# Optimization experiments

Measured on AMD Instinct MI355X. Metric: run time of the kernel, lower is better.

## Reference

```python
import jax, jax.numpy as jnp
import numpy as np

B, T, C = 2, 2048, 1024
H, D = 16, 64


def setup_inputs() -> dict:
    key = jax.random.key(0)
    ks = jax.random.split(key, 5)
    s = 1.0 / np.sqrt(C)  # keep projections well-scaled
    return {
        "x": jax.random.normal(ks[0], (B, T, C), dtype=jnp.float32),
        "wq": jax.random.normal(ks[1], (C, C), dtype=jnp.float32) * s,
        "wk": jax.random.normal(ks[2], (C, C), dtype=jnp.float32) * s,
        "wv": jax.random.normal(ks[3], (C, C), dtype=jnp.float32) * s,
        "wo": jax.random.normal(ks[4], (C, C), dtype=jnp.float32) * s,
    }


def reference(x, wq, wk, wv, wo):
    # nn.Linear(d,d,bias=False): y = x @ W.T ; weights stored [out,in]
    q = (x @ wq.T).reshape(B, T, H, D).transpose(0, 2, 1, 3)  # [B,H,T,D]
    k = (x @ wk.T).reshape(B, T, H, D).transpose(0, 2, 1, 3)
    v = (x @ wv.T).reshape(B, T, H, D).transpose(0, 2, 1, 3)
    scale = jnp.sqrt(jnp.float32(D))
    scores = jnp.einsum("bhtd,bhsd->bhts", q, k) / scale  # [B,H,T,T]
    # additive causal mask: -inf above the diagonal
    causal = jnp.tril(jnp.ones((T, T), dtype=bool))
    scores = jnp.where(causal[None, None], scores, jnp.float32(-1e9))
    weights = jax.nn.softmax(scores, axis=-1)
    out = jnp.einsum("bhts,bhsd->bhtd", weights, v)  # [B,H,T,D]
    out = out.transpose(0, 2, 1, 3).reshape(B, T, C)
    return out @ wo.T
```

## Files before the change

kernel.cpp:

```cpp
#include <hip/hip_runtime.h>
#include <stdint.h>

#define B_ 2
#define T_ 2048
#define C_ 1024
#define H_ 16
#define D_ 64
#define M_ (B_*T_)

typedef __attribute__((ext_vector_type(8))) short bf16x8;
typedef __attribute__((ext_vector_type(4))) short bf16x4;
typedef __attribute__((ext_vector_type(4))) __bf16 bf16v4;
typedef __attribute__((ext_vector_type(4))) float f32x4;
typedef unsigned short u16;

#define MFMA32(a, b, c) __builtin_amdgcn_mfma_f32_16x16x32_bf16((a), (b), (c), 0, 0, 0)

__device__ __forceinline__ u16 f2bf(float f) {
  union { float f; uint32_t u; } v; v.f = f;
  uint32_t u = v.u;
  return (u16)((u + 0x7fffu + ((u >> 16) & 1u)) >> 16);
}

__device__ __forceinline__ float exp2_fast(float x) { return __builtin_amdgcn_exp2f(x); }

typedef const __attribute__((address_space(1))) void* gas_t;
typedef __attribute__((address_space(3))) void* las_t;
__device__ __forceinline__ void gld_lds16(const void* g, void* l) {
  __builtin_amdgcn_global_load_lds((gas_t)g, (las_t)l, 16, 0, 0);
}

__global__ void cvt_all(const float* __restrict__ x,
                        const float* __restrict__ w0, const float* __restrict__ w1,
                        const float* __restrict__ w2, const float* __restrict__ w3,
                        u16* __restrict__ xb,
                        u16* __restrict__ d0, u16* __restrict__ d1,
                        u16* __restrict__ d2, u16* __restrict__ d3) {
  size_t i = ((size_t)blockIdx.x * 256 + threadIdx.x) * 4;
  const float* s; u16* d; size_t off;
  const size_t NX = (size_t)M_ * C_;
  const size_t NW = (size_t)C_ * C_;
  if (i < NX) { s = x; d = xb; off = i; }
  else {
    size_t j = i - NX;
    int w = (int)(j / NW); off = j - (size_t)w * NW;
    switch (w) {
      case 0: s = w0; d = d0; break;
      case 1: s = w1; d = d1; break;
      case 2: s = w2; d = d2; break;
      default: s = w3; d = d3; break;
    }
  }
  float4 v = *(const float4*)(s + off);
  ushort4 o;
  o.x = f2bf(v.x); o.y = f2bf(v.y); o.z = f2bf(v.z); o.w = f2bf(v.w);
  *(ushort4*)(d + off) = o;
}

__device__ __forceinline__ void gemm_core(const u16* __restrict__ A,
                                          const u16* __restrict__ W,
                                          int m0, int n0, int Kt,
                                          f32x4 acc[4][4])
{
  __shared__ u16 As[128*64];
  __shared__ u16 Bs[128*64];
  const int t = threadIdx.x;
  const int lane = t & 63;
  const int wave = t >> 6;
  const int q = lane >> 4;
  const int l15 = lane & 15;
  const int wm = (wave >> 1) * 64;
  const int wn = (wave & 1) * 64;

  #pragma unroll
  for (int i = 0; i < 4; ++i)
    #pragma unroll
    for (int j = 0; j < 4; ++j)
      acc[i][j] = (f32x4){0.f, 0.f, 0.f, 0.f};

  for (int k0 = 0; k0 < Kt; k0 += 64) {
    #pragma unroll
    for (int r = 0; r < 4; ++r) {
      int Lc = r * 256 + t;
      int row = Lc >> 3;
      int gcc = (Lc & 7) ^ (row & 7);
      gld_lds16(A + (size_t)(m0 + row) * Kt + k0 + gcc * 8, As + Lc * 8);
    }
    #pragma unroll
    for (int r = 0; r < 4; ++r) {
      int Lc = r * 256 + t;
      int row = Lc >> 3;
      int gcc = (Lc & 7) ^ (row & 7);
      gld_lds16(W + (size_t)(n0 + row) * Kt + k0 + gcc * 8, Bs + Lc * 8);
    }
    __syncthreads();

    #pragma unroll
    for (int kk = 0; kk < 2; ++kk) {
      bf16x8 af[4], bfr[4];
      #pragma unroll
      for (int i = 0; i < 4; ++i) {
        int m = wm + i * 16 + l15;
        int ch = (kk * 4 + q) ^ (m & 7);
        af[i] = *(const bf16x8*)(As + m * 64 + ch * 8);
      }
      #pragma unroll
      for (int j = 0; j < 4; ++j) {
        int n = wn + j * 16 + l15;
        int ch = (kk * 4 + q) ^ (n & 7);
        bfr[j] = *(const bf16x8*)(Bs + n * 64 + ch * 8);
      }
      #pragma unroll
      for (int i = 0; i < 4; ++i)
        #pragma unroll
        for (int j = 0; j < 4; ++j)
          acc[i][j] = MFMA32(af[i], bfr[j], acc[i][j]);
    }
    __syncthreads();
  }
}

#define QSCALE 0.1803368801111244f
__global__ __launch_bounds__(256, 3)
void gemm_qkv(const u16* __restrict__ X,
              const u16* __restrict__ Wq, const u16* __restrict__ Wk,
              const u16* __restrict__ Wv,
              u16* __restrict__ Q, u16* __restrict__ K, u16* __restrict__ Vt)
{
  const int bm = blockIdx.x;
  const int bn = blockIdx.y;
  const int seg = bn >> 3;
  const int nb = (bn & 7) * 128;

  const int t = threadIdx.x, lane = t & 63, wave = t >> 6;
  const int q = lane >> 4, l15 = lane & 15;
  const int wm = (wave >> 1) * 64, wn = (wave & 1) * 64;

  f32x4 acc[4][4];

  if (seg < 2) {
    const u16* W = (seg == 0) ? Wq : Wk;
    gemm_core(W, X, nb, bm * 128, C_, acc);
    u16* dst = (seg == 0) ? Q : K;
    const float scale = (seg == 0) ? QSCALE : 1.0f;
    #pragma unroll
    for (int i = 0; i < 4; ++i) {
      #pragma unroll
      for (int j = 0; j < 4; ++j) {
        const int o = nb + wm + i * 16 + q * 4;
        const int h = o >> 6, d = o & 63;
        const int mtok = bm * 128 + wn + j * 16 + l15;
        const int b = mtok >> 11, tt = mtok & (T_ - 1);
        ushort4 pk;
        pk.x = f2bf(acc[i][j][0] * scale); pk.y = f2bf(acc[i][j][1] * scale);
        pk.z = f2bf(acc[i][j][2] * scale); pk.w = f2bf(acc[i][j][3] * scale);
        *(ushort4*)(dst + (((size_t)(b * H_ + h)) * T_ + tt) * D_ + d) = pk;
      }
    }
  } else {
    gemm_core(X, Wv, bm * 128, nb, C_, acc);
    #pragma unroll
    for (int i = 0; i < 4; ++i) {
      #pragma unroll
      for (int j = 0; j < 4; ++j) {
        const int mbase = bm * 128 + wm + i * 16 + q * 4;
        const int b = mbase >> 11, tt = mbase & (T_ - 1);
        const int n = nb + wn + j * 16 + l15;
        const int h = n >> 6, d = n & 63;
        const int ttp = (tt & ~31) | ((tt & 12) << 1) | ((tt & 16) >> 2);
        size_t idx = (((size_t)(b * H_ + h)) * D_ + d) * T_ + ttp;
        ushort4 pk;
        pk.x = f2bf(acc[i][j][0]); pk.y = f2bf(acc[i][j][1]);
        pk.z = f2bf(acc[i][j][2]); pk.w = f2bf(acc[i][j][3]);
        *(ushort4*)(Vt + idx) = pk;
      }
    }
  }
}

__global__ __launch_bounds__(512, 2)
void attn(const u16* __restrict__ Q, const u16* __restrict__ K,
          const u16* __restrict__ Vt, u16* __restrict__ Att)
{
  __shared__ u16 SM[32768 + 2048];
  const int t = threadIdx.x;
  const int lane = t & 63, wave = t >> 6;
  const int w4 = wave & 3, wg = wave >> 2;
  const int q = lane >> 4, l15 = lane & 15;
  const int bh = blockIdx.x;
  const int pr = blockIdx.y;
  const int qb0 = pr * 64, qb1 = (15 - pr) * 64;
  const int qb2 = (16 + pr) * 64, qb3 = (31 - pr) * 64;
  int qb[4] = {qb0, qb1, qb2, qb3};
  const u16* Qp = Q + (size_t)bh * T_ * D_;
  const u16* Kp = K + (size_t)bh * T_ * D_;
  const u16* Vp = Vt + (size_t)bh * D_ * T_;

  int rowg[4];
  bf16x8 aq0[4], aq1[4];
  #pragma unroll
  for (int i = 0; i < 4; ++i) {
    rowg[i] = qb[i] + 4 * l15 + w4;
    const u16* qr = Qp + (size_t)rowg[i] * 64;
    aq0[i] = *(const bf16x8*)(qr + q * 8);
    aq1[i] = *(const bf16x8*)(qr + 32 + q * 8);
  }

  f32x4 o[4][4];
  float ls[4];
  #pragma unroll
  for (int i = 0; i < 4; ++i) {
    ls[i] = 0.f;
    #pragma unroll
    for (int j = 0; j < 4; ++j) o[i][j] = (f32x4){0.f, 0.f, 0.f, 0.f};
  }

  auto stage = [&](int kb, int buf) {
    u16* Ksb = SM + buf * 8192;
    u16* Vsb = SM + 16384 + buf * 8192;
    #pragma unroll
    for (int r = 0; r < 2; ++r) {
      int c = r * 512 + t, row = c >> 3, gcc = (c & 7) ^ (row & 7);
      gld_lds16(Kp + (size_t)(kb + row) * 64 + gcc * 8, Ksb + c * 8);
    }
    #pragma unroll
    for (int r = 0; r < 2; ++r) {
      int c = r * 512 + t, row = c >> 4, gcc = (c & 15) ^ (row & 15);
      gld_lds16(Vp + (size_t)row * T_ + kb + gcc * 8, Vsb + c * 8);
    }
  };

  stage(0, 0);
  int cur = 0;
  for (int kb = 0; kb <= qb3; kb += 128, cur ^= 1) {
    __syncthreads();
    if (kb + 128 <= qb3) stage(kb + 128, cur ^ 1);
    const u16* Kc = SM + cur * 8192;
    const u16* Vc = SM + 16384 + cur * 8192;

    const int kbase = kb + wg * 64;
    if (kbase <= qb3) {
      bf16x8 kf0[4], kf1[4];
      #pragma unroll
      for (int j2 = 0; j2 < 4; ++j2) {
        const int rw = wg * 64 + j2 * 16 + l15;
        kf0[j2] = *(const bf16x8*)(Kc + rw * 64 + ((q)     ^ (rw & 7)) * 8);
        kf1[j2] = *(const bf16x8*)(Kc + rw * 64 + ((4 + q) ^ (rw & 7)) * 8);
      }
      bf16x8 vf[4][2];
      #pragma unroll
      for (int j = 0; j < 4; ++j) {
        const int rw = j * 16 + l15;
        #pragma unroll
        for (int kk = 0; kk < 2; ++kk) {
          const int cc = ((2 * wg + kk) * 4 + q) ^ (rw & 15);
          vf[j][kk] = *(const bf16x8*)(Vc + rw * 128 + cc * 8);
        }
      }

      #pragma unroll
      for (int i = 0; i < 4; ++i) {
        if (kbase > qb[i]) continue;
        const bool diag = (kbase == qb[i]);
        bf16x4 pb[4];
        #pragma unroll
        for (int j2 = 0; j2 < 4; ++j2) {
          f32x4 z = (f32x4){0.f, 0.f, 0.f, 0.f};
          __builtin_amdgcn_s_setprio(1);
          z = MFMA32(kf0[j2], aq0[i], z);
          z = MFMA32(kf1[j2], aq1[i], z);
          __builtin_amdgcn_s_setprio(0);
          if (diag) {
            #pragma unroll
            for (int r = 0; r < 4; ++r) {
              const int key = kbase + j2 * 16 + q * 4 + r;
              if (key > rowg[i]) z[r] = -1e30f;
            }
          }
          float p0 = exp2_fast(z[0]), p1 = exp2_fast(z[1]);
          float p2 = exp2_fast(z[2]), p3 = exp2_fast(z[3]);
          ls[i] += (p0 + p1) + (p2 + p3);
          bf16v4 bv;
          bv[0] = (__bf16)p0; bv[1] = (__bf16)p1;
          bv[2] = (__bf16)p2; bv[3] = (__bf16)p3;
          pb[j2] = __builtin_bit_cast(bf16x4, bv);
        }
        __builtin_amdgcn_s_setprio(1);
        #pragma unroll
        for (int kk = 0; kk < 2; ++kk) {
          const bf16x8 pc = __builtin_shufflevector(pb[2 * kk], pb[2 * kk + 1],
                                                    0, 1, 2, 3, 4, 5, 6, 7);
          #pragma unroll
          for (int j = 0; j < 4; ++j)
            o[i][j] = MFMA32(vf[j][kk], pc, o[i][j]);
        }
        __builtin_amdgcn_s_setprio(0);
      }
    }
  }

  __syncthreads();
  float4* red  = (float4*)SM;
  float4* lred = (float4*)(SM + 32768);
  if (wg == 1) {
    #pragma unroll
    for (int i = 0; i < 4; ++i)
      #pragma unroll
      for (int j = 0; j < 4; ++j) {
        float4 v = {o[i][j][0], o[i][j][1], o[i][j][2], o[i][j][3]};
        red[((i * 4 + w4) * 64 + lane) * 4 + j] = v;
      }
    float4 lv = {ls[0], ls[1], ls[2], ls[3]};
    lred[w4 * 64 + lane] = lv;
  }
  __syncthreads();
  if (wg == 0) {
    const float4 lv = lred[w4 * 64 + lane];
    ls[0] += lv.x; ls[1] += lv.y; ls[2] += lv.z; ls[3] += lv.w;
    const int b = bh >> 4, h = bh & 15;
    #pragma unroll
    for (int i = 0; i < 4; ++i) {
      #pragma unroll
      for (int j = 0; j < 4; ++j) {
        const float4 v = red[((i * 4 + w4) * 64 + lane) * 4 + j];
        o[i][j][0] += v.x; o[i][j][1] += v.y;
        o[i][j][2] += v.z; o[i][j][3] += v.w;
      }
      float l = ls[i];
      l += __shfl_xor(l, 16, 64); l += __shfl_xor(l, 32, 64);
      const float inv = __builtin_amdgcn_rcpf(l);
      #pragma unroll
      for (int j = 0; j < 4; ++j) {
        ushort4 pk;
        pk.x = f2bf(o[i][j][0] * inv); pk.y = f2bf(o[i][j][1] * inv);
        pk.z = f2bf(o[i][j][2] * inv); pk.w = f2bf(o[i][j][3] * inv);
        *(ushort4*)(Att + ((size_t)b * T_ + rowg[i]) * C_ + h * 64 + j * 16 + q * 4) = pk;
      }
    }
  }
}

__global__ __launch_bounds__(256, 2)
void gemm_out(const u16* __restrict__ Att, const u16* __restrict__ Wo,
              float* __restrict__ Out)
{
  __shared__ u16 As[64 * 64];
  __shared__ u16 Bs[128 * 64];
  const int t = threadIdx.x;
  const int lane = t & 63, wave = t >> 6;
  const int q = lane >> 4, l15 = lane & 15;
  const int wm = (wave >> 1) * 32, wn = (wave & 1) * 64;
  const int m0 = blockIdx.x * 64;
  const int n0 = blockIdx.y * 128;

  f32x4 acc[2][4];
  #pragma unroll
  for (int i = 0; i < 2; ++i)
    #pragma unroll
    for (int j = 0; j < 4; ++j)
      acc[i][j] = (f32x4){0.f, 0.f, 0.f, 0.f};

  for (int k0 = 0; k0 < C_; k0 += 64) {
    #pragma unroll
    for (int r = 0; r < 2; ++r) {
      int Lc = r * 256 + t, row = Lc >> 3, gcc = (Lc & 7) ^ (row & 7);
      gld_lds16(Wo + (size_t)(m0 + row) * C_ + k0 + gcc * 8, As + Lc * 8);
    }
    #pragma unroll
    for (int r = 0; r < 4; ++r) {
      int Lc = r * 256 + t, row = Lc >> 3, gcc = (Lc & 7) ^ (row & 7);
      gld_lds16(Att + (size_t)(n0 + row) * C_ + k0 + gcc * 8, Bs + Lc * 8);
    }
    __syncthreads();

    #pragma unroll
    for (int kk = 0; kk < 2; ++kk) {
      bf16x8 af[2], bfr[4];
      #pragma unroll
      for (int i = 0; i < 2; ++i) {
        int m = wm + i * 16 + l15;
        int ch = (kk * 4 + q) ^ (m & 7);
        af[i] = *(const bf16x8*)(As + m * 64 + ch * 8);
      }
      #pragma unroll
      for (int j = 0; j < 4; ++j) {
        int n = wn + j * 16 + l15;
        int ch = (kk * 4 + q) ^ (n & 7);
        bfr[j] = *(const bf16x8*)(Bs + n * 64 + ch * 8);
      }
      #pragma unroll
      for (int i = 0; i < 2; ++i)
        #pragma unroll
        for (int j = 0; j < 4; ++j)
          acc[i][j] = MFMA32(af[i], bfr[j], acc[i][j]);
    }
    __syncthreads();
  }

  #pragma unroll
  for (int i = 0; i < 2; ++i) {
    #pragma unroll
    for (int j = 0; j < 4; ++j) {
      const int o = m0 + wm + i * 16 + q * 4;
      const int tok = n0 + wn + j * 16 + l15;
      float4 st = {acc[i][j][0], acc[i][j][1], acc[i][j][2], acc[i][j][3]};
      *(float4*)(Out + (size_t)tok * C_ + o) = st;
    }
  }
}

extern "C" void kernel_launch(void* const* d_in, const int* in_sizes, int n_in,
                              void* d_out, int out_size, void* d_ws, size_t ws_size,
                              hipStream_t stream) {
  const float* x  = (const float*)d_in[0];
  const float* wq = (const float*)d_in[1];
  const float* wk = (const float*)d_in[2];
  const float* wv = (const float*)d_in[3];
  const float* wo = (const float*)d_in[4];
  float* out = (float*)d_out;

  u16* ws  = (u16*)d_ws;
  u16* xb  = ws;
  u16* wqb = xb  + (size_t)M_ * C_;
  u16* wkb = wqb + (size_t)C_ * C_;
  u16* wvb = wkb + (size_t)C_ * C_;
  u16* wob = wvb + (size_t)C_ * C_;
  u16* Qb  = wob + (size_t)C_ * C_;
  u16* Kb  = Qb  + (size_t)M_ * C_;
  u16* Vtb = Kb  + (size_t)M_ * C_;
  u16* Atb = Vtb + (size_t)M_ * C_;

  cvt_all<<<dim3((M_ * C_ + 4 * C_ * C_) / 1024), 256, 0, stream>>>(
      x, wq, wk, wv, wo, xb, wqb, wkb, wvb, wob);

  gemm_qkv<<<dim3(M_ / 128, 24), 256, 0, stream>>>(xb, wqb, wkb, wvb, Qb, Kb, Vtb);
  attn<<<dim3(B_ * H_, 8), 512, 0, stream>>>(Qb, Kb, Vtb, Atb);
  gemm_out<<<dim3(C_ / 64, M_ / 128), 256, 0, stream>>>(Atb, wob, out);
}
```

Measured before the change: 157.5 us.

## Fuse Q and K projections into one block sharing the X tile

Q and K projection tiles are now computed together in the same block. Each X tile staged in LDS feeds both the Wq and Wk MFMA streams, which cuts redundant X loads and reduces the grid from 24 to 16 column blocks. Shared memory is hoisted into the kernel and the V path reuses it. The cost is twice the accumulator registers on the fused path, and launch bounds drop from 3 to 2 blocks per CU. The grid also becomes unbalanced: fused Q/K blocks do twice the work of V blocks.

After: 161.4 us. 2.5% more time.

```diff
diff --git a/kernel.cpp b/kernel.cpp
--- a/kernel.cpp
+++ b/kernel.cpp
@@ -60,10 +60,9 @@
 __device__ __forceinline__ void gemm_core(const u16* __restrict__ A,
                                           const u16* __restrict__ W,
                                           int m0, int n0, int Kt,
-                                          f32x4 acc[4][4])
+                                          f32x4 acc[4][4],
+                                          u16* As, u16* Bs)
 {
-  __shared__ u16 As[128*64];
-  __shared__ u16 Bs[128*64];
   const int t = threadIdx.x;
   const int lane = t & 63;
   const int wave = t >> 6;
@@ -121,28 +120,75 @@
 }
 
 #define QSCALE 0.1803368801111244f
-__global__ __launch_bounds__(256, 3)
+__global__ __launch_bounds__(256, 2)
 void gemm_qkv(const u16* __restrict__ X,
               const u16* __restrict__ Wq, const u16* __restrict__ Wk,
               const u16* __restrict__ Wv,
               u16* __restrict__ Q, u16* __restrict__ K, u16* __restrict__ Vt)
 {
+  __shared__ u16 SMA[128 * 64];
+  __shared__ u16 SMB[128 * 64];
+  __shared__ u16 SMC[128 * 64];
   const int bm = blockIdx.x;
   const int bn = blockIdx.y;
-  const int seg = bn >> 3;
-  const int nb = (bn & 7) * 128;
+  const int seg = bn & 1;
+  const int nb = (bn >> 1) * 128;
 
   const int t = threadIdx.x, lane = t & 63, wave = t >> 6;
   const int q = lane >> 4, l15 = lane & 15;
   const int wm = (wave >> 1) * 64, wn = (wave & 1) * 64;
 
-  f32x4 acc[4][4];
-
-  if (seg < 2) {
-    const u16* W = (seg == 0) ? Wq : Wk;
-    gemm_core(W, X, nb, bm * 128, C_, acc);
-    u16* dst = (seg == 0) ? Q : K;
-    const float scale = (seg == 0) ? QSCALE : 1.0f;
+  if (seg == 0) {
+    f32x4 aq[4][4], ak[4][4];
+    #pragma unroll
+    for (int i = 0; i < 4; ++i)
+      #pragma unroll
+      for (int j = 0; j < 4; ++j) {
+        aq[i][j] = (f32x4){0.f, 0.f, 0.f, 0.f};
+        ak[i][j] = (f32x4){0.f, 0.f, 0.f, 0.f};
+      }
+
+    const int m0 = nb;
+    const int n0 = bm * 128;
+    for (int k0 = 0; k0 < C_; k0 += 64) {
+      #pragma unroll
+      for (int r = 0; r < 4; ++r) {
+        int Lc = r * 256 + t;
+        int row = Lc >> 3;
+        int gcc = (Lc & 7) ^ (row & 7);
+        gld_lds16(Wq + (size_t)(m0 + row) * C_ + k0 + gcc * 8, SMA + Lc * 8);
+        gld_lds16(Wk + (size_t)(m0 + row) * C_ + k0 + gcc * 8, SMB + Lc * 8);
+        gld_lds16(X  + (size_t)(n0 + row) * C_ + k0 + gcc * 8, SMC + Lc * 8);
+      }
+      __syncthreads();
+
+      #pragma unroll
+      for (int kk = 0; kk < 2; ++kk) {
+        bf16x8 afq[4], afk[4], bfr[4];
+        #pragma unroll
+        for (int i = 0; i < 4; ++i) {
+          int m = wm + i * 16 + l15;
+          int ch = (kk * 4 + q) ^ (m & 7);
+          afq[i] = *(const bf16x8*)(SMA + m * 64 + ch * 8);
+          afk[i] = *(const bf16x8*)(SMB + m * 64 + ch * 8);
+        }
+        #pragma unroll
+        for (int j = 0; j < 4; ++j) {
+          int n = wn + j * 16 + l15;
+          int ch = (kk * 4 + q) ^ (n & 7);
+          bfr[j] = *(const bf16x8*)(SMC + n * 64 + ch * 8);
+        }
+        #pragma unroll
+        for (int i = 0; i < 4; ++i)
+          #pragma unroll
+          for (int j = 0; j < 4; ++j) {
+            aq[i][j] = MFMA32(afq[i], bfr[j], aq[i][j]);
+            ak[i][j] = MFMA32(afk[i], bfr[j], ak[i][j]);
+          }
+      }
+      __syncthreads();
+    }
+
     #pragma unroll
     for (int i = 0; i < 4; ++i) {
       #pragma unroll
@@ -151,14 +197,19 @@
         const int h = o >> 6, d = o & 63;
         const int mtok = bm * 128 + wn + j * 16 + l15;
         const int b = mtok >> 11, tt = mtok & (T_ - 1);
-        ushort4 pk;
-        pk.x = f2bf(acc[i][j][0] * scale); pk.y = f2bf(acc[i][j][1] * scale);
-        pk.z = f2bf(acc[i][j][2] * scale); pk.w = f2bf(acc[i][j][3] * scale);
-        *(ushort4*)(dst + (((size_t)(b * H_ + h)) * T_ + tt) * D_ + d) = pk;
+        const size_t idx = (((size_t)(b * H_ + h)) * T_ + tt) * D_ + d;
+        ushort4 pq, pk;
+        pq.x = f2bf(aq[i][j][0] * QSCALE); pq.y = f2bf(aq[i][j][1] * QSCALE);
+        pq.z = f2bf(aq[i][j][2] * QSCALE); pq.w = f2bf(aq[i][j][3] * QSCALE);
+        pk.x = f2bf(ak[i][j][0]); pk.y = f2bf(ak[i][j][1]);
+        pk.z = f2bf(ak[i][j][2]); pk.w = f2bf(ak[i][j][3]);
+        *(ushort4*)(Q + idx) = pq;
+        *(ushort4*)(K + idx) = pk;
       }
     }
   } else {
-    gemm_core(X, Wv, bm * 128, nb, C_, acc);
+    f32x4 acc[4][4];
+    gemm_core(X, Wv, bm * 128, nb, C_, acc, SMA, SMB);
     #pragma unroll
     for (int i = 0; i < 4; ++i) {
       #pragma unroll
@@ -433,7 +484,7 @@
   cvt_all<<<dim3((M_ * C_ + 4 * C_ * C_) / 1024), 256, 0, stream>>>(
       x, wq, wk, wv, wo, xb, wqb, wkb, wvb, wob);
 
-  gemm_qkv<<<dim3(M_ / 128, 24), 256, 0, stream>>>(xb, wqb, wkb, wvb, Qb, Kb, Vtb);
+  gemm_qkv<<<dim3(M_ / 128, 16), 256, 0, stream>>>(xb, wqb, wkb, wvb, Qb, Kb, Vtb);
   attn<<<dim3(B_ * H_, 8), 512, 0, stream>>>(Qb, Kb, Vtb, Atb);
   gemm_out<<<dim3(C_ / 64, M_ / 128), 256, 0, stream>>>(Atb, wob, out);
 }
```
